# Performance work log

Measured on AMD Instinct MI355X. Metric: run time of the kernel, lower is better.

Reference implementation:

```python
import jax, jax.numpy as jnp
import numpy as np

B, S = 4, 128          # batch, seq
IN, OUT = 1024, 1024   # perfect squares
C = 256                # compressed_feature_dim
K = 4                  # num_monarchs
NI, NO = 32, 32        # sqrt(IN), sqrt(OUT)
D1 = NI * NI * NO      # flat size of M1 per token
D2 = NO * NI * NO      # flat size of M2 per token


def setup_inputs() -> dict:
    key = jax.random.key(0)
    ks = jax.random.split(key, 20)
    s = 0.02
    return {
        "x":   jax.random.normal(ks[0], (B, S, IN), dtype=jnp.float32),
        # compressor: Linear(IN, C)
        "Wc":  jax.random.normal(ks[1], (IN, C), dtype=jnp.float32) * s,
        "bc":  jnp.zeros((C,), dtype=jnp.float32),
        # M1 generators (stacked over K experts): Linear(C,C), SiLU, Linear(C,D1)
        "W1a": jax.random.normal(ks[2], (K, C, C), dtype=jnp.float32) * s,
        "b1a": jnp.zeros((K, C), dtype=jnp.float32),
        "W1b": jax.random.normal(ks[3], (K, C, D1), dtype=jnp.float32) * s,
        "b1b": jax.random.normal(ks[4], (K, D1), dtype=jnp.float32) * s,
        # M2 generators
        "W2a": jax.random.normal(ks[5], (K, C, C), dtype=jnp.float32) * s,
        "b2a": jnp.zeros((K, C), dtype=jnp.float32),
        "W2b": jax.random.normal(ks[6], (K, C, D2), dtype=jnp.float32) * s,
        "b2b": jax.random.normal(ks[7], (K, D2), dtype=jnp.float32) * s,
        # mixer: Linear(C,C), SiLU, Linear(C,K)
        "Wm1": jax.random.normal(ks[8], (C, C), dtype=jnp.float32) * s,
        "bm1": jnp.zeros((C,), dtype=jnp.float32),
        "Wm2": jax.random.normal(ks[9], (C, K), dtype=jnp.float32) * s,
        "bm2": jnp.zeros((K,), dtype=jnp.float32),
        # biasor: Linear(C, OUT)
        "Wb":  jax.random.normal(ks[10], (C, OUT), dtype=jnp.float32) * s,
        "bb":  jnp.zeros((OUT,), dtype=jnp.float32),
        # ratio_gen: Linear(C, 1)
        "Wr":  jax.random.normal(ks[11], (C, 1), dtype=jnp.float32) * s,
        "br":  jnp.ones((1,), dtype=jnp.float32),
    }


def reference(x, Wc, bc, W1a, b1a, W1b, b1b, W2a, b2a, W2b, b2b,
              Wm1, bm1, Wm2, bm2, Wb, bb, Wr, br):
    silu = jax.nn.silu
    # compressor
    c = silu(x @ Wc + bc)                                   # [B,S,C]
    # per-expert hypernetwork generation of flat Monarch factors
    h1 = silu(jnp.einsum('bsc,kcd->kbsd', c, W1a) + b1a[:, None, None, :])
    M1s = jnp.einsum('kbsd,kde->kbse', h1, W1b) + b1b[:, None, None, :]  # [K,B,S,D1]
    h2 = silu(jnp.einsum('bsc,kcd->kbsd', c, W2a) + b2a[:, None, None, :])
    M2s = jnp.einsum('kbsd,kde->kbse', h2, W2b) + b2b[:, None, None, :]  # [K,B,S,D2]
    # softmax mixing coefficients
    coeffs = jax.nn.softmax(silu(c @ Wm1 + bm1) @ Wm2 + bm2, axis=-1)    # [B,S,K]
    M1_flat = jnp.einsum('kbsd,bsk->bsd', M1s, coeffs)      # [B,S,D1]
    M2_flat = jnp.einsum('kbsd,bsk->bsd', M2s, coeffs)      # [B,S,D2]
    # per-token Monarch matmul
    lead = x.shape[:-1]
    M1 = M1_flat.reshape(*lead, NI, NI, NO)
    M2 = M2_flat.reshape(*lead, NO, NI, NO)
    x1 = x.reshape(*lead, NI, NI)                            # [B,S,g=NI,i=NI]
    x1o = jnp.einsum('bsgi,bsgio->bsgo', x1, M1)             # [B,S,NI,NO]
    x2 = jnp.swapaxes(x1o, -1, -2)                           # [B,S,NO,NI]
    x2o = jnp.einsum('bsgi,bsgio->bsgo', x2, M2)             # [B,S,NO,NO]
    y = x2o.reshape(*lead, NO * NO)                          # [B,S,OUT]
    ratio = c @ Wr + br                                      # [B,S,1]
    return y * ratio + (c @ Wb + bb)
```

## Files before the change

### kernel.cpp

```cpp
#include <hip/hip_runtime.h>


typedef __bf16 bf16x8 __attribute__((ext_vector_type(8)));
typedef __bf16 bf16x2 __attribute__((ext_vector_type(2)));
typedef float  fx4    __attribute__((ext_vector_type(4)));

#define NN 32768

__device__ __forceinline__ unsigned short f2bf(float f) {
  union { __bf16 b; unsigned short u; } c; c.b = (__bf16)f; return c.u;
}
__device__ __forceinline__ unsigned pk2(float lo, float hi) {
  bf16x2 v; v[0] = (__bf16)lo; v[1] = (__bf16)hi;
  union { bf16x2 v; unsigned u; } c; c.v = v; return c.u;
}
__device__ __forceinline__ float b2f(unsigned short s) {
  union { unsigned u; float f; } v; v.u = ((unsigned)s) << 16; return v.f;
}
__device__ __forceinline__ void up8(uint4 h, float* f) {
  f[0] = b2f((unsigned short)(h.x & 0xFFFF)); f[1] = b2f((unsigned short)(h.x >> 16));
  f[2] = b2f((unsigned short)(h.y & 0xFFFF)); f[3] = b2f((unsigned short)(h.y >> 16));
  f[4] = b2f((unsigned short)(h.z & 0xFFFF)); f[5] = b2f((unsigned short)(h.z >> 16));
  f[6] = b2f((unsigned short)(h.w & 0xFFFF)); f[7] = b2f((unsigned short)(h.w >> 16));
}
__device__ __forceinline__ uint4 scale8(uint4 h, float cv) {
  uint4 u;
  u.x = pk2(b2f((unsigned short)(h.x & 0xFFFF)) * cv, b2f((unsigned short)(h.x >> 16)) * cv);
  u.y = pk2(b2f((unsigned short)(h.y & 0xFFFF)) * cv, b2f((unsigned short)(h.y >> 16)) * cv);
  u.z = pk2(b2f((unsigned short)(h.z & 0xFFFF)) * cv, b2f((unsigned short)(h.z >> 16)) * cv);
  u.w = pk2(b2f((unsigned short)(h.w & 0xFFFF)) * cv, b2f((unsigned short)(h.w >> 16)) * cv);
  return u;
}
__device__ __forceinline__ float silu_f(float x) { return x / (1.f + __expf(-x)); }

__device__ __forceinline__ void gl2lds16(const void* g, void* l) {
  __builtin_amdgcn_global_load_lds(
      (const __attribute__((address_space(1))) unsigned int*)g,
      (__attribute__((address_space(3))) unsigned int*)l, 16, 0, 0);
}

#define MFMA(a, b, c) __builtin_amdgcn_mfma_f32_16x16x32_bf16((a), (b), (c), 0, 0, 0)

__device__ __forceinline__ void wconv_body(int cb, const float* __restrict__ W,
                                           const float* __restrict__ bvec,
                                           uint4* __restrict__ Wt) {
  const int ur = cb >> 5;
  const int n0 = (cb & 31) * 1024 + threadIdx.x * 4;
  fx4 r[8];
  if (ur < 128) {
#pragma unroll
    for (int kk = 0; kk < 8; ++kk)
      r[kk] = *(const fx4*)(W + (size_t)(ur * 8 + kk) * NN + n0);
  } else {
#pragma unroll
    for (int kk = 0; kk < 8; ++kk) r[kk] = 0;
    if (ur == 128) {
#pragma unroll
      for (int kk = 0; kk < 4; ++kk)
        r[kk] = *(const fx4*)(bvec + (size_t)kk * NN + n0);
    }
  }
#pragma unroll
  for (int j = 0; j < 4; ++j) {
    uint4 u;
    u.x = pk2(r[0][j], r[1][j]); u.y = pk2(r[2][j], r[3][j]);
    u.z = pk2(r[4][j], r[5][j]); u.w = pk2(r[6][j], r[7][j]);
    Wt[(size_t)ur * NN + n0 + j] = u;
  }
}

__global__ __launch_bounds__(256) void k1_compress(
    const float* __restrict__ x, const float* __restrict__ Wc,
    const float* __restrict__ bc, uint4* __restrict__ c_u4,
    const float* __restrict__ W1b, const float* __restrict__ b1b,
    uint4* __restrict__ Wt) {
  const int b = blockIdx.x;
  if (b >= 32) { wconv_body(b - 32, W1b, b1b, Wt); return; }
  const int tid = threadIdx.x;
  const int m0 = (b & 7) * 64, n0 = (b >> 3) * 64;
  __shared__ uint4 As[8 * 64];
  __shared__ uint4 Bs[8 * 65];
  const bf16x8* Af = reinterpret_cast<const bf16x8*>(As);
  const bf16x8* Bf = reinterpret_cast<const bf16x8*>(Bs);
  uint2* Bs2 = reinterpret_cast<uint2*>(Bs);
  const int lane = tid & 63, w = tid >> 6;
  const int q = lane >> 4, rr = lane & 15;
  const int wm = (w >> 1) * 32, wn = (w & 1) * 32;
  const int arun = tid & 7, amb = tid >> 3;
  const int kgrp = tid & 15, colg = tid >> 4;
  fx4 a00 = 0, a01 = 0, a10 = 0, a11 = 0;
  fx4 areg[4], breg[4];

#pragma unroll
  for (int s = 0; s < 2; ++s) {
    const float* src = x + (size_t)(m0 + amb + 32 * s) * 1024 + arun * 8;
    areg[2 * s] = *(const fx4*)src;
    areg[2 * s + 1] = *(const fx4*)(src + 4);
  }
#pragma unroll
  for (int kk = 0; kk < 4; ++kk)
    breg[kk] = *(const fx4*)(Wc + (size_t)(kgrp * 4 + kk) * 256 + n0 + colg * 4);

  for (int kt = 0; kt < 16; ++kt) {
    __syncthreads();
#pragma unroll
    for (int s = 0; s < 2; ++s) {
      uint4 u;
      u.x = pk2(areg[2 * s][0], areg[2 * s][1]);
      u.y = pk2(areg[2 * s][2], areg[2 * s][3]);
      u.z = pk2(areg[2 * s + 1][0], areg[2 * s + 1][1]);
      u.w = pk2(areg[2 * s + 1][2], areg[2 * s + 1][3]);
      As[arun * 64 + amb + 32 * s] = u;
    }
#pragma unroll
    for (int j = 0; j < 4; ++j) {
      uint2 u;
      u.x = pk2(breg[0][j], breg[1][j]);
      u.y = pk2(breg[2][j], breg[3][j]);
      Bs2[(((kgrp >> 1) * 65 + colg * 4 + j) << 1) + (kgrp & 1)] = u;
    }
    __syncthreads();
    if (kt < 15) {
      const int k0 = (kt + 1) * 64;
#pragma unroll
      for (int s = 0; s < 2; ++s) {
        const float* src = x + (size_t)(m0 + amb + 32 * s) * 1024 + k0 + arun * 8;
        areg[2 * s] = *(const fx4*)src;
        areg[2 * s + 1] = *(const fx4*)(src + 4);
      }
#pragma unroll
      for (int kk = 0; kk < 4; ++kk)
        breg[kk] = *(const fx4*)(Wc + (size_t)(k0 + kgrp * 4 + kk) * 256 + n0 + colg * 4);
    }
#pragma unroll
    for (int ks = 0; ks < 2; ++ks) {
      const int roA = (ks * 4 + q) * 64, roB = (ks * 4 + q) * 65;
      bf16x8 fa0 = Af[roA + wm + rr];
      bf16x8 fa1 = Af[roA + wm + 16 + rr];
      bf16x8 fb0 = Bf[roB + wn + rr];
      bf16x8 fb1 = Bf[roB + wn + 16 + rr];
      a00 = MFMA(fa0, fb0, a00); a01 = MFMA(fa0, fb1, a01);
      a10 = MFMA(fa1, fb0, a10); a11 = MFMA(fa1, fb1, a11);
    }
  }
  __syncthreads();
  {
    const int r4 = tid >> 6, m = tid & 63;
    uint4 u; u.x = (r4 == 0) ? 0x3F80u : 0u; u.y = 0; u.z = 0; u.w = 0;
    As[r4 * 64 + m] = u;
    uint4 ub; ub.x = (r4 == 0) ? (unsigned)f2bf(bc[n0 + m]) : 0u;
    ub.y = 0; ub.z = 0; ub.w = 0;
    Bs[r4 * 65 + m] = ub;
  }
  __syncthreads();
  {
    bf16x8 fa0 = Af[q * 64 + wm + rr];
    bf16x8 fa1 = Af[q * 64 + wm + 16 + rr];
    bf16x8 fb0 = Bf[q * 65 + wn + rr];
    bf16x8 fb1 = Bf[q * 65 + wn + 16 + rr];
    a00 = MFMA(fa0, fb0, a00); a01 = MFMA(fa0, fb1, a01);
    a10 = MFMA(fa1, fb0, a10); a11 = MFMA(fa1, fb1, a11);
  }
  unsigned short* c16 = (unsigned short*)c_u4;
#pragma unroll
  for (int fi = 0; fi < 2; ++fi) {
#pragma unroll
    for (int fj = 0; fj < 2; ++fj) {
      fx4 v = (fi == 0) ? (fj == 0 ? a00 : a01) : (fj == 0 ? a10 : a11);
      const int cc = n0 + wn + fj * 16 + rr;
#pragma unroll
      for (int reg = 0; reg < 4; ++reg) {
        const int t = m0 + wm + fi * 16 + q * 4 + reg;
        c16[((size_t)(cc >> 3) * 512 + t) * 8 + (cc & 7)] = f2bf(silu_f(v[reg]));
      }
    }
  }
  if ((b >> 3) == 0) {
    const int r4 = tid >> 6, m = tid & 63;
    uint4 u; u.x = (r4 == 0) ? 0x3F80u : 0u; u.y = 0; u.z = 0; u.w = 0;
    c_u4[(size_t)(32 + r4) * 512 + m0 + m] = u;
  }
}

__global__ __launch_bounds__(256) void k2_hyper(
    const uint4* __restrict__ c_u4,
    const float* __restrict__ W1a, const float* __restrict__ b1a,
    const float* __restrict__ W2a, const float* __restrict__ b2a,
    const float* __restrict__ Wm1, const float* __restrict__ bm1,
    const float* __restrict__ Wb, const float* __restrict__ bb,
    unsigned short* __restrict__ H, float* __restrict__ biasout) {
  const int tid = threadIdx.x;
  const int m0 = blockIdx.x * 64, n0 = blockIdx.y * 64;
  __shared__ uint4 As[2][8 * 64];
  __shared__ uint4 Bs[8 * 65];
  const bf16x8* Bf = reinterpret_cast<const bf16x8*>(Bs);
  uint2* Bs2 = reinterpret_cast<uint2*>(Bs);
  const int lane = tid & 63, w = tid >> 6;
  const int q = lane >> 4, rr = lane & 15;
  const int wm = (w >> 1) * 32, wn = (w & 1) * 32;
  const int kgrp = tid & 15, colg = tid >> 4;

  const float* bbase; const float* biasv; int bstride;
  if (n0 < 1024) {
    const int kx = n0 >> 8;
    bbase = W1a + (size_t)kx * 65536 + (n0 & 255); bstride = 256;
    biasv = b1a + kx * 256 + (n0 & 255);
  } else if (n0 < 2048) {
    const int mm = n0 - 1024; const int kx = mm >> 8;
    bbase = W2a + (size_t)kx * 65536 + (mm & 255); bstride = 256;
    biasv = b2a + kx * 256 + (mm & 255);
  } else if (n0 < 2304) {
    bbase = Wm1 + (n0 - 2048); bstride = 256; biasv = bm1 + (n0 - 2048);
  } else {
    bbase = Wb + (n0 - 2304); bstride = 1024; biasv = bb + (n0 - 2304);
  }

  fx4 a00 = 0, a01 = 0, a10 = 0, a11 = 0;
  fx4 breg[4];
#pragma unroll
  for (int kk = 0; kk < 4; ++kk)
    breg[kk] = *(const fx4*)(bbase + (size_t)(kgrp * 4 + kk) * bstride + colg * 4);
#pragma unroll
  for (int s = 0; s < 2; ++s) {
    const int run = w * 2 + s;
    gl2lds16(c_u4 + (size_t)run * 512 + m0 + lane, (void*)(&As[0][run * 64]));
  }
  int cur = 0;
  for (int kt = 0; kt < 4; ++kt) {
    __syncthreads();
#pragma unroll
    for (int j = 0; j < 4; ++j) {
      uint2 u;
      u.x = pk2(breg[0][j], breg[1][j]);
      u.y = pk2(breg[2][j], breg[3][j]);
      Bs2[(((kgrp >> 1) * 65 + colg * 4 + j) << 1) + (kgrp & 1)] = u;
    }
    __syncthreads();
    if (kt < 3) {
#pragma unroll
      for (int s = 0; s < 2; ++s) {
        const int run = w * 2 + s;
        gl2lds16(c_u4 + (size_t)((kt + 1) * 8 + run) * 512 + m0 + lane,
                 (void*)(&As[cur ^ 1][run * 64]));
      }
#pragma unroll
      for (int kk = 0; kk < 4; ++kk)
        breg[kk] = *(const fx4*)(bbase + (size_t)((kt + 1) * 64 + kgrp * 4 + kk) * bstride + colg * 4);
    }
    const bf16x8* Af = reinterpret_cast<const bf16x8*>(As[cur]);
#pragma unroll
    for (int ks = 0; ks < 2; ++ks) {
      const int roA = (ks * 4 + q) * 64, roB = (ks * 4 + q) * 65;
      bf16x8 fa0 = Af[roA + wm + rr];
      bf16x8 fa1 = Af[roA + wm + 16 + rr];
      bf16x8 fb0 = Bf[roB + wn + rr];
      bf16x8 fb1 = Bf[roB + wn + 16 + rr];
      a00 = MFMA(fa0, fb0, a00); a01 = MFMA(fa0, fb1, a01);
      a10 = MFMA(fa1, fb0, a10); a11 = MFMA(fa1, fb1, a11);
    }
    cur ^= 1;
  }
  __syncthreads();
  {
    gl2lds16(c_u4 + (size_t)(32 + w) * 512 + m0 + lane, (void*)(&As[0][w * 64]));
    const int r4 = tid >> 6, col = tid & 63;
    uint4 ub; ub.x = (r4 == 0) ? (unsigned)f2bf(biasv[col]) : 0u;
    ub.y = 0; ub.z = 0; ub.w = 0;
    Bs[r4 * 65 + col] = ub;
  }
  __syncthreads();
  {
    const bf16x8* Af = reinterpret_cast<const bf16x8*>(As[0]);
    bf16x8 fa0 = Af[q * 64 + wm + rr];
    bf16x8 fa1 = Af[q * 64 + wm + 16 + rr];
    bf16x8 fb0 = Bf[q * 65 + wn + rr];
    bf16x8 fb1 = Bf[q * 65 + wn + 16 + rr];
    a00 = MFMA(fa0, fb0, a00); a01 = MFMA(fa0, fb1, a01);
    a10 = MFMA(fa1, fb0, a10); a11 = MFMA(fa1, fb1, a11);
  }
#pragma unroll
  for (int fi = 0; fi < 2; ++fi) {
#pragma unroll
    for (int fj = 0; fj < 2; ++fj) {
      fx4 v = (fi == 0) ? (fj == 0 ? a00 : a01) : (fj == 0 ? a10 : a11);
      const int cc = n0 + wn + fj * 16 + rr;
#pragma unroll
      for (int reg = 0; reg < 4; ++reg) {
        const int t = m0 + wm + fi * 16 + q * 4 + reg;
        if (n0 < 2304)
          H[(((size_t)(cc >> 3) * 512 + t) << 3) + (cc & 7)] = f2bf(silu_f(v[reg]));
        else
          biasout[(size_t)t * 1024 + (cc - 2304)] = v[reg];
      }
    }
  }
}

__global__ __launch_bounds__(256) void k3_prep(
    const uint4* __restrict__ Hu, const uint4* __restrict__ c_u4,
    const float* __restrict__ Wm2, const float* __restrict__ bm2,
    const float* __restrict__ Wr, const float* __restrict__ br,
    uint4* __restrict__ G1u, uint4* __restrict__ G2u, float* __restrict__ ratio) {
  const int tid = threadIdx.x;
  const int tg = blockIdx.x & 7, dgrp = blockIdx.x >> 3;
  const int t0 = tg * 64;
  __shared__ float sWm2[1024];
  __shared__ float sWr[256];
  __shared__ float part[64][4][4];
  __shared__ float rp[64][4];
  __shared__ float cf[64][4];
  ((fx4*)sWm2)[tid] = ((const fx4*)Wm2)[tid];
  if (tid < 64) ((fx4*)sWr)[tid] = ((const fx4*)Wr)[tid];
  __syncthreads();
  const int tl = tid >> 2, kx = tid & 3;
  {
    float pe0 = 0, pe1 = 0, pe2 = 0, pe3 = 0, pr = 0;
#pragma unroll
    for (int i = 0; i < 8; ++i) {
      uint4 h  = Hu[(size_t)(256 + kx * 8 + i) * 512 + t0 + tl];
      uint4 cu = c_u4[(size_t)(kx * 8 + i) * 512 + t0 + tl];
      float hf[8], cv[8];
      up8(h, hf); up8(cu, cv);
#pragma unroll
      for (int j = 0; j < 8; ++j) {
        const int ch = kx * 64 + i * 8 + j;
        pe0 += hf[j] * sWm2[ch * 4 + 0];
        pe1 += hf[j] * sWm2[ch * 4 + 1];
        pe2 += hf[j] * sWm2[ch * 4 + 2];
        pe3 += hf[j] * sWm2[ch * 4 + 3];
        pr  += cv[j] * sWr[ch];
      }
    }
    part[tl][kx][0] = pe0; part[tl][kx][1] = pe1;
    part[tl][kx][2] = pe2; part[tl][kx][3] = pe3;
    rp[tl][kx] = pr;
  }
  __syncthreads();
  if (tid < 64) {
    float l[4];
#pragma unroll
    for (int e = 0; e < 4; ++e)
      l[e] = part[tid][0][e] + part[tid][1][e] + part[tid][2][e] + part[tid][3][e] + bm2[e];
    float m = fmaxf(fmaxf(l[0], l[1]), fmaxf(l[2], l[3]));
    float e0 = __expf(l[0] - m), e1 = __expf(l[1] - m);
    float e2 = __expf(l[2] - m), e3 = __expf(l[3] - m);
    float den = e0 + e1 + e2 + e3;
    cf[tid][0] = e0 / den; cf[tid][1] = e1 / den;
    cf[tid][2] = e2 / den; cf[tid][3] = e3 / den;
    if (dgrp == 0)
      ratio[t0 + tid] = rp[tid][0] + rp[tid][1] + rp[tid][2] + rp[tid][3] + br[0];
  }
  __syncthreads();
  const int tl2 = tid & 63, sub = tid >> 6;
#pragma unroll
  for (int i = 0; i < 4; ++i) {
    const int dg = dgrp * 16 + sub * 4 + i;
    const float cv = cf[tl2][dg >> 5];
    uint4 h1 = Hu[(size_t)dg * 512 + t0 + tl2];
    G1u[(size_t)dg * 512 + t0 + tl2] = scale8(h1, cv);
    uint4 h2 = Hu[(size_t)(128 + dg) * 512 + t0 + tl2];
    G2u[(size_t)dg * 512 + t0 + tl2] = scale8(h2, cv);
  }
  if (dgrp == 0) {
    if (tid < 64) {
      uint4 u;
      u.x = pk2(cf[tid][0], cf[tid][1]);
      u.y = pk2(cf[tid][2], cf[tid][3]);
      u.z = 0; u.w = 0;
      G1u[(size_t)128 * 512 + t0 + tid] = u;
      G2u[(size_t)128 * 512 + t0 + tid] = u;
    } else {
      const int idx = tid - 64;
      uint4 z; z.x = 0; z.y = 0; z.z = 0; z.w = 0;
      G1u[(size_t)(129 + (idx >> 6)) * 512 + t0 + (idx & 63)] = z;
      G2u[(size_t)(129 + (idx >> 6)) * 512 + t0 + (idx & 63)] = z;
    }
  }
}

__global__ __launch_bounds__(256) void k_biggemm(
    const uint4* __restrict__ Gu, const uint4* __restrict__ Wt,
    unsigned short* __restrict__ Mout) {
  const int tid = threadIdx.x;
  const int p = blockIdx.x;
  const int xcd = p & 7, slot = p >> 3;
  const int m0 = (slot & 3) * 128;
  const int n0 = ((slot >> 2) * 8 + xcd) * 128;
  __shared__ uint4 As[8 * 128];
  __shared__ uint4 Bs[8 * 128];
  const bf16x8* Af = reinterpret_cast<const bf16x8*>(As);
  const bf16x8* Bf = reinterpret_cast<const bf16x8*>(Bs);
  const int lane = tid & 63, w = tid >> 6;
  const int q = lane >> 4, rr = lane & 15;
  const int wm = (w >> 1) * 64, wn = (w & 1) * 64;

  fx4 acc[4][4];
#pragma unroll
  for (int i = 0; i < 4; ++i)
#pragma unroll
    for (int j = 0; j < 4; ++j) acc[i][j] = 0;

  for (int kt = 0; kt < 16; ++kt) {
    __syncthreads();
#pragma unroll
    for (int s = 0; s < 4; ++s) {
      const int idx = w * 4 + s;
      const int run = idx >> 1, hf = (idx & 1) * 64;
      gl2lds16(Gu + (size_t)(kt * 8 + run) * 512 + m0 + hf + lane,
               (void*)(&As[run * 128 + hf]));
      gl2lds16(Wt + (size_t)(kt * 8 + run) * NN + n0 + hf + lane,
               (void*)(&Bs[run * 128 + hf]));
    }
    __syncthreads();
#pragma unroll
    for (int ks = 0; ks < 2; ++ks) {
      const int ro = (ks * 4 + q) * 128;
      bf16x8 a[4], b[4];
#pragma unroll
      for (int f = 0; f < 4; ++f) {
        a[f] = Af[ro + wm + f * 16 + rr];
        b[f] = Bf[ro + wn + f * 16 + rr];
      }
#pragma unroll
      for (int fi = 0; fi < 4; ++fi)
#pragma unroll
        for (int fj = 0; fj < 4; ++fj) acc[fi][fj] = MFMA(a[fi], b[fj], acc[fi][fj]);
    }
  }
  __syncthreads();
#pragma unroll
  for (int s = 0; s < 2; ++s) {
    const int idx = w * 2 + s;
    const int run = idx >> 1, hf = (idx & 1) * 64;
    gl2lds16(Gu + (size_t)(128 + run) * 512 + m0 + hf + lane,
             (void*)(&As[run * 128 + hf]));
    gl2lds16(Wt + (size_t)(128 + run) * NN + n0 + hf + lane,
             (void*)(&Bs[run * 128 + hf]));
  }
  __syncthreads();
  {
    const int ro = q * 128;
    bf16x8 a[4], b[4];
#pragma unroll
    for (int f = 0; f < 4; ++f) {
      a[f] = Af[ro + wm + f * 16 + rr];
      b[f] = Bf[ro + wn + f * 16 + rr];
    }
#pragma unroll
    for (int fi = 0; fi < 4; ++fi)
#pragma unroll
      for (int fj = 0; fj < 4; ++fj) acc[fi][fj] = MFMA(a[fi], b[fj], acc[fi][fj]);
  }
#pragma unroll
  for (int fi = 0; fi < 4; ++fi) {
    const int tb = m0 + wm + fi * 16 + q * 4;
#pragma unroll
    for (int fj = 0; fj < 4; ++fj) {
      const fx4 v = acc[fi][fj];
      const int cc = n0 + wn + fj * 16 + rr;
      const int pc = ((cc >> 5) & 31) * 1024 + (cc >> 10) * 32 + (cc & 31);
#pragma unroll
      for (int reg = 0; reg < 4; ++reg)
        Mout[(size_t)(tb + reg) * NN + pc] = f2bf(v[reg]);
    }
  }
}

__global__ __launch_bounds__(256) void k_monarch1(
    const float* __restrict__ x, const unsigned short* __restrict__ M1p,
    float* __restrict__ XT,
    const float* __restrict__ W2b, const float* __restrict__ b2b,
    uint4* __restrict__ Wt) {
  const int b = blockIdx.x;
  if (b >= 512) { wconv_body(b - 512, W2b, b2b, Wt); return; }
  const int tt = b, tid = threadIdx.x;
  const int h = tid >> 7, t2 = tid & 127;
  __shared__ float xs[1024];
  __shared__ float xo[2][1024];
  *(float4*)&xs[tid * 4] = *(const float4*)&x[(size_t)tt * 1024 + tid * 4];
  __syncthreads();
  const int g = t2 >> 2, ob = (t2 & 3) * 8;
  const unsigned short* mrow =
      M1p + (size_t)tt * NN + (size_t)h * 16 * 1024 + g * 32 + ob;
  float acc[8] = {0, 0, 0, 0, 0, 0, 0, 0};
#pragma unroll
  for (int i = 0; i < 16; ++i) {
    uint4 mv = *(const uint4*)&mrow[(size_t)i * 1024];
    float mf[8]; up8(mv, mf);
    const float xv = xs[g * 32 + h * 16 + i];
#pragma unroll
    for (int j = 0; j < 8; ++j) acc[j] += xv * mf[j];
  }
#pragma unroll
  for (int j = 0; j < 8; ++j) xo[h][(ob + j) * 32 + g] = acc[j];
  __syncthreads();
  {
    const int base = tid * 4;
    float4 v0 = *(const float4*)&xo[0][base];
    float4 v1 = *(const float4*)&xo[1][base];
    float4 o; o.x = v0.x + v1.x; o.y = v0.y + v1.y;
    o.z = v0.z + v1.z; o.w = v0.w + v1.w;
    *(float4*)&XT[(size_t)tt * 1024 + base] = o;
  }
}

__global__ __launch_bounds__(256) void k_monarch2(
    const unsigned short* __restrict__ M2p, const float* __restrict__ XT,
    const float* __restrict__ biasout, const float* __restrict__ ratio,
    float* __restrict__ out) {
  const int tt = blockIdx.x, tid = threadIdx.x;
  const int h = tid >> 7, t2 = tid & 127;
  __shared__ float xs[1024];
  __shared__ float xo[2][1024];
  *(float4*)&xs[tid * 4] = *(const float4*)&XT[(size_t)tt * 1024 + tid * 4];
  __syncthreads();
  const int g = t2 >> 2, ob = (t2 & 3) * 8;
  const unsigned short* mrow =
      M2p + (size_t)tt * NN + (size_t)h * 16 * 1024 + g * 32 + ob;
  float acc[8] = {0, 0, 0, 0, 0, 0, 0, 0};
#pragma unroll
  for (int i = 0; i < 16; ++i) {
    uint4 mv = *(const uint4*)&mrow[(size_t)i * 1024];
    float mf[8]; up8(mv, mf);
    const float xv = xs[g * 32 + h * 16 + i];
#pragma unroll
    for (int j = 0; j < 8; ++j) acc[j] += xv * mf[j];
  }
#pragma unroll
  for (int j = 0; j < 8; ++j) xo[h][g * 32 + ob + j] = acc[j];
  __syncthreads();
  {
    const float r = ratio[tt];
    const int base = tid * 4;
    float4 v0 = *(const float4*)&xo[0][base];
    float4 v1 = *(const float4*)&xo[1][base];
    float4 bo = *(const float4*)&biasout[(size_t)tt * 1024 + base];
    float4 o;
    o.x = (v0.x + v1.x) * r + bo.x; o.y = (v0.y + v1.y) * r + bo.y;
    o.z = (v0.z + v1.z) * r + bo.z; o.w = (v0.w + v1.w) * r + bo.w;
    *(float4*)&out[(size_t)tt * 1024 + base] = o;
  }
}

extern "C" void kernel_launch(void* const* d_in, const int* in_sizes, int n_in,
                              void* d_out, int out_size, void* d_ws, size_t ws_size,
                              hipStream_t stream) {
  (void)in_sizes; (void)n_in; (void)out_size; (void)ws_size;
  const float* x   = (const float*)d_in[0];
  const float* Wc  = (const float*)d_in[1];
  const float* bc  = (const float*)d_in[2];
  const float* W1a = (const float*)d_in[3];
  const float* b1a = (const float*)d_in[4];
  const float* W1b = (const float*)d_in[5];
  const float* b1b = (const float*)d_in[6];
  const float* W2a = (const float*)d_in[7];
  const float* b2a = (const float*)d_in[8];
  const float* W2b = (const float*)d_in[9];
  const float* b2b = (const float*)d_in[10];
  const float* Wm1 = (const float*)d_in[11];
  const float* bm1 = (const float*)d_in[12];
  const float* Wm2 = (const float*)d_in[13];
  const float* bm2 = (const float*)d_in[14];
  const float* Wb  = (const float*)d_in[15];
  const float* bb  = (const float*)d_in[16];
  const float* Wr  = (const float*)d_in[17];
  const float* br  = (const float*)d_in[18];
  float* out = (float*)d_out;

  char* ws = (char*)d_ws;
  uint4* c_u4            = (uint4*)(ws + 0);
  unsigned short* H      = (unsigned short*)(ws + 294912);
  float* biasout         = (float*)(ws + 2654208);
  uint4* G1u             = (uint4*)(ws + 4751360);
  uint4* G2u             = (uint4*)(ws + 5832704);
  float* ratio           = (float*)(ws + 6914048);
  float* XT              = (float*)(ws + 6918144);
  unsigned short* M      = (unsigned short*)(ws + 9015296);
  uint4* Wt              = (uint4*)(ws + 42569728);

  k1_compress<<<4256, 256, 0, stream>>>(x, Wc, bc, c_u4, W1b, b1b, Wt);
  k2_hyper<<<dim3(8, 52), 256, 0, stream>>>(c_u4, W1a, b1a, W2a, b2a, Wm1, bm1,
                                            Wb, bb, H, biasout);
  k3_prep<<<64, 256, 0, stream>>>((const uint4*)H, c_u4, Wm2, bm2, Wr, br,
                                  G1u, G2u, ratio);
  k_biggemm<<<1024, 256, 0, stream>>>(G1u, Wt, M);
  k_monarch1<<<4736, 256, 0, stream>>>(x, M, XT, W2b, b2b, Wt);
  k_biggemm<<<1024, 256, 0, stream>>>(G2u, Wt, M);
  k_monarch2<<<512, 256, 0, stream>>>(M, XT, biasout, ratio, out);
}
```

Before: 441.2 us.

## Fuse Monarch contraction into generator GEMM epilogue with atomic accumulation

The per-token Monarch contractions now run inside the epilogue of the big hypernetwork GEMM, so the bf16 M1/M2 factors are never written to global memory. Each tile scales its accumulators by the matching x entries staged in shared memory, reduces partials through LDS, and atomically adds into zero-initialised X1/Y buffers. The W2b conversion moves from the monarch1 kernel into k2_hyper, and a small final kernel applies ratio and bias. This removes a large write and reread of the generated factors, at the cost of float atomics (non-deterministic summation order), an extra zeroing pass and a larger workspace holding both converted weight sets.

```diff
diff --git a/kernel.cpp b/kernel.cpp
--- a/kernel.cpp
+++ b/kernel.cpp
@@ -73,9 +73,9 @@
     const float* __restrict__ x, const float* __restrict__ Wc,
     const float* __restrict__ bc, uint4* __restrict__ c_u4,
     const float* __restrict__ W1b, const float* __restrict__ b1b,
-    uint4* __restrict__ Wt) {
+    uint4* __restrict__ Wt1) {
   const int b = blockIdx.x;
-  if (b >= 32) { wconv_body(b - 32, W1b, b1b, Wt); return; }
+  if (b >= 32) { wconv_body(b - 32, W1b, b1b, Wt1); return; }
   const int tid = threadIdx.x;
   const int m0 = (b & 7) * 64, n0 = (b >> 3) * 64;
   __shared__ uint4 As[8 * 64];
@@ -188,9 +188,13 @@
     const float* __restrict__ W2a, const float* __restrict__ b2a,
     const float* __restrict__ Wm1, const float* __restrict__ bm1,
     const float* __restrict__ Wb, const float* __restrict__ bb,
-    unsigned short* __restrict__ H, float* __restrict__ biasout) {
+    unsigned short* __restrict__ H, float* __restrict__ biasout,
+    const float* __restrict__ W2b, const float* __restrict__ b2b,
+    uint4* __restrict__ Wt2) {
+  const int b = blockIdx.x;
+  if (b >= 416) { wconv_body(b - 416, W2b, b2b, Wt2); return; }
   const int tid = threadIdx.x;
-  const int m0 = blockIdx.x * 64, n0 = blockIdx.y * 64;
+  const int m0 = (b & 7) * 64, n0 = (b >> 3) * 64;
   __shared__ uint4 As[2][8 * 64];
   __shared__ uint4 Bs[8 * 65];
   const bf16x8* Bf = reinterpret_cast<const bf16x8*>(Bs);
@@ -300,9 +304,18 @@
     const uint4* __restrict__ Hu, const uint4* __restrict__ c_u4,
     const float* __restrict__ Wm2, const float* __restrict__ bm2,
     const float* __restrict__ Wr, const float* __restrict__ br,
-    uint4* __restrict__ G1u, uint4* __restrict__ G2u, float* __restrict__ ratio) {
+    uint4* __restrict__ G1u, uint4* __restrict__ G2u, float* __restrict__ ratio,
+    float* __restrict__ X1, float* __restrict__ Y) {
+  const int b = blockIdx.x;
   const int tid = threadIdx.x;
-  const int tg = blockIdx.x & 7, dgrp = blockIdx.x >> 3;
+  if (b >= 64) {
+    const int zb = b - 64;
+    float* dst = (zb < 64 ? X1 : Y) + (size_t)(zb & 63) * 8192;
+#pragma unroll
+    for (int r2 = 0; r2 < 8; ++r2) ((fx4*)dst)[r2 * 256 + tid] = 0;
+    return;
+  }
+  const int tg = b & 7, dgrp = b >> 3;
   const int t0 = tg * 64;
   __shared__ float sWm2[1024];
   __shared__ float sWr[256];
@@ -378,21 +391,38 @@
   }
 }
 
-__global__ __launch_bounds__(256) void k_biggemm(
+__global__ __launch_bounds__(256) void k_biggemm_fused(
     const uint4* __restrict__ Gu, const uint4* __restrict__ Wt,
-    unsigned short* __restrict__ Mout) {
+    const float* __restrict__ xsrc, float* __restrict__ Xout, const int mode) {
   const int tid = threadIdx.x;
   const int p = blockIdx.x;
   const int xcd = p & 7, slot = p >> 3;
   const int m0 = (slot & 3) * 128;
   const int n0 = ((slot >> 2) * 8 + xcd) * 128;
-  __shared__ uint4 As[8 * 128];
-  __shared__ uint4 Bs[8 * 128];
+  const int g_blk = n0 >> 10;
+  const int i0 = (n0 >> 5) & 31;
+  __shared__ uint4 smem[2048];
+  __shared__ float sx[4 * 128];
+  uint4* As = smem;
+  uint4* Bs = smem + 1024;
   const bf16x8* Af = reinterpret_cast<const bf16x8*>(As);
   const bf16x8* Bf = reinterpret_cast<const bf16x8*>(Bs);
   const int lane = tid & 63, w = tid >> 6;
   const int q = lane >> 4, rr = lane & 15;
   const int wm = (w >> 1) * 64, wn = (w & 1) * 64;
+
+  if (tid < 128) {
+    if (mode == 0) {
+      fx4 v = *(const fx4*)(xsrc + (size_t)(m0 + tid) * 1024 + g_blk * 32 + i0);
+      sx[0 * 128 + tid] = v[0]; sx[1 * 128 + tid] = v[1];
+      sx[2 * 128 + tid] = v[2]; sx[3 * 128 + tid] = v[3];
+    } else {
+#pragma unroll
+      for (int ii = 0; ii < 4; ++ii)
+        sx[ii * 128 + tid] =
+            xsrc[(size_t)(m0 + tid) * 1024 + (i0 + ii) * 32 + g_blk];
+    }
+  }
 
   fx4 acc[4][4];
 #pragma unroll
@@ -451,95 +481,45 @@
 #pragma unroll
       for (int fj = 0; fj < 4; ++fj) acc[fi][fj] = MFMA(a[fi], b[fj], acc[fi][fj]);
   }
+
+  __syncthreads();
+  float* part = (float*)smem;
+  const int ip = wn >> 5;
+  const int hbase = (w & 1) * 4096;
 #pragma unroll
   for (int fi = 0; fi < 4; ++fi) {
-    const int tb = m0 + wm + fi * 16 + q * 4;
-#pragma unroll
-    for (int fj = 0; fj < 4; ++fj) {
-      const fx4 v = acc[fi][fj];
-      const int cc = n0 + wn + fj * 16 + rr;
-      const int pc = ((cc >> 5) & 31) * 1024 + (cc >> 10) * 32 + (cc & 31);
-#pragma unroll
-      for (int reg = 0; reg < 4; ++reg)
-        Mout[(size_t)(tb + reg) * NN + pc] = f2bf(v[reg]);
-    }
-  }
-}
-
-__global__ __launch_bounds__(256) void k_monarch1(
-    const float* __restrict__ x, const unsigned short* __restrict__ M1p,
-    float* __restrict__ XT,
-    const float* __restrict__ W2b, const float* __restrict__ b2b,
-    uint4* __restrict__ Wt) {
-  const int b = blockIdx.x;
-  if (b >= 512) { wconv_body(b - 512, W2b, b2b, Wt); return; }
-  const int tt = b, tid = threadIdx.x;
-  const int h = tid >> 7, t2 = tid & 127;
-  __shared__ float xs[1024];
-  __shared__ float xo[2][1024];
-  *(float4*)&xs[tid * 4] = *(const float4*)&x[(size_t)tt * 1024 + tid * 4];
-  __syncthreads();
-  const int g = t2 >> 2, ob = (t2 & 3) * 8;
-  const unsigned short* mrow =
-      M1p + (size_t)tt * NN + (size_t)h * 16 * 1024 + g * 32 + ob;
-  float acc[8] = {0, 0, 0, 0, 0, 0, 0, 0};
-#pragma unroll
-  for (int i = 0; i < 16; ++i) {
-    uint4 mv = *(const uint4*)&mrow[(size_t)i * 1024];
-    float mf[8]; up8(mv, mf);
-    const float xv = xs[g * 32 + h * 16 + i];
-#pragma unroll
-    for (int j = 0; j < 8; ++j) acc[j] += xv * mf[j];
-  }
-#pragma unroll
-  for (int j = 0; j < 8; ++j) xo[h][(ob + j) * 32 + g] = acc[j];
-  __syncthreads();
-  {
-    const int base = tid * 4;
-    float4 v0 = *(const float4*)&xo[0][base];
-    float4 v1 = *(const float4*)&xo[1][base];
-    float4 o; o.x = v0.x + v1.x; o.y = v0.y + v1.y;
-    o.z = v0.z + v1.z; o.w = v0.w + v1.w;
-    *(float4*)&XT[(size_t)tt * 1024 + base] = o;
-  }
-}
-
-__global__ __launch_bounds__(256) void k_monarch2(
-    const unsigned short* __restrict__ M2p, const float* __restrict__ XT,
-    const float* __restrict__ biasout, const float* __restrict__ ratio,
-    float* __restrict__ out) {
-  const int tt = blockIdx.x, tid = threadIdx.x;
-  const int h = tid >> 7, t2 = tid & 127;
-  __shared__ float xs[1024];
-  __shared__ float xo[2][1024];
-  *(float4*)&xs[tid * 4] = *(const float4*)&XT[(size_t)tt * 1024 + tid * 4];
-  __syncthreads();
-  const int g = t2 >> 2, ob = (t2 & 3) * 8;
-  const unsigned short* mrow =
-      M2p + (size_t)tt * NN + (size_t)h * 16 * 1024 + g * 32 + ob;
-  float acc[8] = {0, 0, 0, 0, 0, 0, 0, 0};
-#pragma unroll
-  for (int i = 0; i < 16; ++i) {
-    uint4 mv = *(const uint4*)&mrow[(size_t)i * 1024];
-    float mf[8]; up8(mv, mf);
-    const float xv = xs[g * 32 + h * 16 + i];
-#pragma unroll
-    for (int j = 0; j < 8; ++j) acc[j] += xv * mf[j];
-  }
-#pragma unroll
-  for (int j = 0; j < 8; ++j) xo[h][g * 32 + ob + j] = acc[j];
-  __syncthreads();
-  {
-    const float r = ratio[tt];
-    const int base = tid * 4;
-    float4 v0 = *(const float4*)&xo[0][base];
-    float4 v1 = *(const float4*)&xo[1][base];
-    float4 bo = *(const float4*)&biasout[(size_t)tt * 1024 + base];
-    float4 o;
-    o.x = (v0.x + v1.x) * r + bo.x; o.y = (v0.y + v1.y) * r + bo.y;
-    o.z = (v0.z + v1.z) * r + bo.z; o.w = (v0.w + v1.w) * r + bo.w;
-    *(float4*)&out[(size_t)tt * 1024 + base] = o;
-  }
+#pragma unroll
+    for (int reg = 0; reg < 4; ++reg) {
+      const int tl = wm + fi * 16 + q * 4 + reg;
+      const float s0 = sx[ip * 128 + tl], s1 = sx[(ip + 1) * 128 + tl];
+      part[hbase + tl * 32 + rr] =
+          acc[fi][0][reg] * s0 + acc[fi][2][reg] * s1;
+      part[hbase + tl * 32 + rr + 16] =
+          acc[fi][1][reg] * s0 + acc[fi][3][reg] * s1;
+    }
+  }
+  __syncthreads();
+#pragma unroll
+  for (int r2 = 0; r2 < 16; ++r2) {
+    const int idx = tid + r2 * 256;
+    const int tl = idx >> 5, o = idx & 31;
+    const float v = part[idx] + part[4096 + idx];
+    atomicAdd(&Xout[(size_t)(m0 + tl) * 1024 + g_blk * 32 + o], v);
+  }
+}
+
+__global__ __launch_bounds__(256) void k_final(
+    const float* __restrict__ Y, const float* __restrict__ ratio,
+    const float* __restrict__ biasout, float* __restrict__ out) {
+  const int t = blockIdx.x, tid = threadIdx.x;
+  const float r = ratio[t];
+  const int base = tid * 4;
+  float4 y  = *(const float4*)&Y[(size_t)t * 1024 + base];
+  float4 bo = *(const float4*)&biasout[(size_t)t * 1024 + base];
+  float4 o;
+  o.x = y.x * r + bo.x; o.y = y.y * r + bo.y;
+  o.z = y.z * r + bo.z; o.w = y.w * r + bo.w;
+  *(float4*)&out[(size_t)t * 1024 + base] = o;
 }
 
 extern "C" void kernel_launch(void* const* d_in, const int* in_sizes, int n_in,
@@ -574,17 +554,17 @@
   uint4* G1u             = (uint4*)(ws + 4751360);
   uint4* G2u             = (uint4*)(ws + 5832704);
   float* ratio           = (float*)(ws + 6914048);
-  float* XT              = (float*)(ws + 6918144);
-  unsigned short* M      = (unsigned short*)(ws + 9015296);
-  uint4* Wt              = (uint4*)(ws + 42569728);
-
-  k1_compress<<<4256, 256, 0, stream>>>(x, Wc, bc, c_u4, W1b, b1b, Wt);
-  k2_hyper<<<dim3(8, 52), 256, 0, stream>>>(c_u4, W1a, b1a, W2a, b2a, Wm1, bm1,
-                                            Wb, bb, H, biasout);
-  k3_prep<<<64, 256, 0, stream>>>((const uint4*)H, c_u4, Wm2, bm2, Wr, br,
-                                  G1u, G2u, ratio);
-  k_biggemm<<<1024, 256, 0, stream>>>(G1u, Wt, M);
-  k_monarch1<<<4736, 256, 0, stream>>>(x, M, XT, W2b, b2b, Wt);
-  k_biggemm<<<1024, 256, 0, stream>>>(G2u, Wt, M);
-  k_monarch2<<<512, 256, 0, stream>>>(M, XT, biasout, ratio, out);
-}
+  float* X1              = (float*)(ws + 6918144);
+  float* Y               = (float*)(ws + 9015296);
+  uint4* Wt1             = (uint4*)(ws + 11112448);
+  uint4* Wt2             = (uint4*)(ws + 80318464);
+
+  k1_compress<<<4256, 256, 0, stream>>>(x, Wc, bc, c_u4, W1b, b1b, Wt1);
+  k2_hyper<<<4640, 256, 0, stream>>>(c_u4, W1a, b1a, W2a, b2a, Wm1, bm1,
+                                     Wb, bb, H, biasout, W2b, b2b, Wt2);
+  k3_prep<<<192, 256, 0, stream>>>((const uint4*)H, c_u4, Wm2, bm2, Wr, br,
+                                   G1u, G2u, ratio, X1, Y);
+  k_biggemm_fused<<<1024, 256, 0, stream>>>(G1u, Wt1, x, X1, 0);
+  k_biggemm_fused<<<1024, 256, 0, stream>>>(G2u, Wt2, X1, Y, 1);
+  k_final<<<512, 256, 0, stream>>>(Y, ratio, biasout, out);
+}
```

After: 459.6 us. 4.2% more time.
